# Performance work log

Measured on AMD Instinct MI355X. Metric: run time of the kernel, lower is better.

## Reference

```python
import jax, jax.numpy as jnp
import numpy as np

D = 512       # model_dim
H = 8         # num_heads
DH = D // H   # dim_per_head
LN_EPS = 1e-5


def setup_inputs() -> dict:
    key = jax.random.key(0)
    ks = jax.random.split(key, 10)
    B, S = 2, 2048
    s = D ** -0.5
    return {
        "query": jax.random.normal(ks[0], (B, S, D), jnp.float32),
        "key":   jax.random.normal(ks[1], (B, S, D), jnp.float32),
        "value": jax.random.normal(ks[2], (B, S, D), jnp.float32),
        # torch Linear weights: [out, in], y = x @ W.T
        "Wq": jax.random.normal(ks[3], (D, D), jnp.float32) * s,
        "Wk": jax.random.normal(ks[4], (D, D), jnp.float32) * s,
        "Wv": jax.random.normal(ks[5], (D, D), jnp.float32) * s,
        "Wo": jax.random.normal(ks[6], (D, D), jnp.float32) * s,
        "bo": jnp.zeros((D,), jnp.float32),
        "gamma": jnp.ones((D,), jnp.float32),
        "beta":  jnp.zeros((D,), jnp.float32),
    }


def _layer_norm(x, gamma, beta):
    mu = jnp.mean(x, axis=-1, keepdims=True)
    var = jnp.var(x, axis=-1, keepdims=True)
    return (x - mu) * jax.lax.rsqrt(var + LN_EPS) * gamma + beta


def reference(query, key, value, Wq, Wk, Wv, Wo, bo, gamma, beta):
    B, S, _ = query.shape
    residual = query
    # projections (torch Linear: x @ W.T), split heads -> [B, H, S, DH]
    q = (query @ Wq.T).reshape(B, S, H, DH).transpose(0, 2, 1, 3)
    k = (key   @ Wk.T).reshape(B, S, H, DH).transpose(0, 2, 1, 3)
    v = (value @ Wv.T).reshape(B, S, H, DH).transpose(0, 2, 1, 3)
    scale = DH ** -0.5
    scores = jnp.einsum('bhqd,bhkd->bhqk', q, k) * scale
    attention = jax.nn.softmax(scores, axis=-1)
    context = jnp.einsum('bhqk,bhkd->bhqd', attention, v)
    context = context.transpose(0, 2, 1, 3).reshape(B, S, D)
    output = context @ Wo.T + bo
    output = _layer_norm(residual + output, gamma, beta)
    # original returns attention as [B*H, S, S]
    return output, attention.reshape(B * H, S, S)
```

## Files before the change

### kernel.cpp

```cpp
#include <hip/hip_runtime.h>

#define B_ 2
#define S_ 2048
#define D_ 512
#define H_ 8
#define DH_ 64

typedef __bf16 bf16_8 __attribute__((ext_vector_type(8)));
typedef float f32x4 __attribute__((ext_vector_type(4)));
typedef unsigned int u32x4 __attribute__((ext_vector_type(4)));

union BfPack4 { ushort4 u; __bf16 h[4]; };

__global__ __launch_bounds__(256) void proj_qkv(
    const float* __restrict__ Xq, const float* __restrict__ Xk, const float* __restrict__ Xv,
    const float* __restrict__ Wq, const float* __restrict__ Wk, const float* __restrict__ Wv,
    __bf16* __restrict__ Qb, __bf16* __restrict__ Kb, __bf16* __restrict__ Vt)
{
    const int z = blockIdx.z;
    const float* X = (z == 0) ? Xq : (z == 1) ? Xk : Xv;
    const float* W = (z == 0) ? Wq : (z == 1) ? Wk : Wv;
    const int m0 = blockIdx.x * 64;
    const int n0 = blockIdx.y * 64;

    __shared__ __bf16 Xs[64][72];
    __shared__ __bf16 Ws[64][72];

    const int tid = threadIdx.x;
    const int w = tid >> 6, lane = tid & 63;
    const int quad = lane >> 4, mc = lane & 15;

    int rr[4], cc[4];
    for (int i = 0; i < 4; ++i) { int e = tid + i * 256; rr[i] = e >> 4; cc[i] = (e & 15) * 4; }

    f32x4 acc[4] = {};
    float4 xr[4], wv[4];
    for (int i = 0; i < 4; ++i) {
        xr[i] = *reinterpret_cast<const float4*>(&X[(size_t)(m0 + rr[i]) * 512 + cc[i]]);
        wv[i] = *reinterpret_cast<const float4*>(&W[(size_t)(n0 + rr[i]) * 512 + cc[i]]);
    }

    for (int kc = 0; kc < 512; kc += 64) {
        if (kc) __syncthreads();
        for (int i = 0; i < 4; ++i) {
            BfPack4 px, pw;
            px.h[0] = (__bf16)xr[i].x; px.h[1] = (__bf16)xr[i].y;
            px.h[2] = (__bf16)xr[i].z; px.h[3] = (__bf16)xr[i].w;
            *reinterpret_cast<ushort4*>(&Xs[rr[i]][cc[i]]) = px.u;
            pw.h[0] = (__bf16)wv[i].x; pw.h[1] = (__bf16)wv[i].y;
            pw.h[2] = (__bf16)wv[i].z; pw.h[3] = (__bf16)wv[i].w;
            *reinterpret_cast<ushort4*>(&Ws[rr[i]][cc[i]]) = pw.u;
        }
        __syncthreads();
        if (kc < 448) {
            for (int i = 0; i < 4; ++i) {
                xr[i] = *reinterpret_cast<const float4*>(&X[(size_t)(m0 + rr[i]) * 512 + kc + 64 + cc[i]]);
                wv[i] = *reinterpret_cast<const float4*>(&W[(size_t)(n0 + rr[i]) * 512 + kc + 64 + cc[i]]);
            }
        }
        for (int ks = 0; ks < 64; ks += 32) {
            bf16_8 a = *reinterpret_cast<const bf16_8*>(&Xs[w * 16 + mc][ks + quad * 8]);
            for (int tt = 0; tt < 4; ++tt) {
                bf16_8 bb = *reinterpret_cast<const bf16_8*>(&Ws[tt * 16 + mc][ks + quad * 8]);
                acc[tt] = __builtin_amdgcn_mfma_f32_16x16x32_bf16(a, bb, acc[tt], 0, 0, 0);
            }
        }
    }
    __syncthreads();
    const float scale = (z == 0) ? 0.125f : 1.0f;
    if (z < 2) {
        for (int tt = 0; tt < 4; ++tt)
            for (int r = 0; r < 4; ++r)
                Xs[w * 16 + quad * 4 + r][tt * 16 + mc] = (__bf16)(acc[tt][r] * scale);
    } else {
        for (int tt = 0; tt < 4; ++tt)
            for (int r = 0; r < 4; ++r)
                Xs[tt * 16 + mc][w * 16 + quad * 4 + r] = (__bf16)acc[tt][r];
    }
    __syncthreads();
    if (z < 2) {
        __bf16* out = (z == 0) ? Qb : Kb;
        for (int i = 0; i < 2; ++i) {
            int e = tid + i * 256;
            int r = e >> 3, c8 = (e & 7) * 8;
            *reinterpret_cast<uint4*>(&out[(size_t)(m0 + r) * 512 + n0 + c8]) =
                *reinterpret_cast<const uint4*>(&Xs[r][c8]);
        }
    } else {
        int b = m0 >> 11, s0 = m0 & 2047, h = n0 >> 6;
        for (int i = 0; i < 2; ++i) {
            int e = tid + i * 256;
            int r = e >> 3, c8 = (e & 7) * 8;
            *reinterpret_cast<uint4*>(&Vt[(((size_t)(b * H_ + h)) * DH_ + r) * S_ + s0 + c8]) =
                *reinterpret_cast<const uint4*>(&Xs[r][c8]);
        }
    }
}

__global__ __launch_bounds__(256) void attn_kernel(
    const __bf16* __restrict__ Qb, const __bf16* __restrict__ Kb, const __bf16* __restrict__ Vt,
    __bf16* __restrict__ Ctx, float* __restrict__ attn_out)
{
    const int qt = blockIdx.x;
    const int bh = blockIdx.y;
    const int b = bh >> 3, h = bh & 7;
    const int q0 = qt * 16;

    __shared__ __align__(16) char smem[4 * 16 * 528 * 2];
    __shared__ float Lsh[4][16];

    const int tid = threadIdx.x;
    const int kg = tid >> 6, lane = tid & 63;
    const int quad = lane >> 4, mc = lane & 15;

    __bf16* PsW = reinterpret_cast<__bf16*>(smem) + (size_t)kg * 16 * 528;

    const __bf16* qrow = &Qb[((size_t)b * S_ + q0 + mc) * D_ + h * DH_];
    const bf16_8 aq0 = *reinterpret_cast<const bf16_8*>(&qrow[quad * 8]);
    const bf16_8 aq1 = *reinterpret_cast<const bf16_8*>(&qrow[32 + quad * 8]);

    const __bf16* kbase = Kb + ((size_t)b * S_ + kg * 512) * D_ + h * DH_;
    const __bf16* vbase = Vt + (size_t)bh * DH_ * S_ + kg * 512;

    float l[4] = {0.f, 0.f, 0.f, 0.f};
    f32x4 o[4] = {};

    for (int c = 0; c < 8; ++c) {
        const __bf16* kc_ = kbase + (size_t)c * 64 * D_;
        bf16_8 kb[8];
        for (int tt = 0; tt < 4; ++tt)
            kb[tt] = *reinterpret_cast<const bf16_8*>(&kc_[(size_t)(tt * 16 + mc) * D_ + quad * 8]);
        for (int tt = 0; tt < 4; ++tt)
            kb[4 + tt] = *reinterpret_cast<const bf16_8*>(&kc_[(size_t)(tt * 16 + mc) * D_ + 32 + quad * 8]);
        f32x4 s[4] = {};
        for (int tt = 0; tt < 4; ++tt)
            s[tt] = __builtin_amdgcn_mfma_f32_16x16x32_bf16(aq0, kb[tt], s[tt], 0, 0, 0);
        for (int tt = 0; tt < 4; ++tt)
            s[tt] = __builtin_amdgcn_mfma_f32_16x16x32_bf16(aq1, kb[4 + tt], s[tt], 0, 0, 0);
        for (int tt = 0; tt < 4; ++tt)
            for (int j = 0; j < 4; ++j) {
                float p = __expf(s[tt][j]);
                l[j] += p;
                PsW[(size_t)(quad * 4 + j) * 528 + c * 64 + tt * 16 + mc] = (__bf16)p;
            }
        bf16_8 vb[8];
        for (int ks2 = 0; ks2 < 2; ++ks2)
            for (int tt = 0; tt < 4; ++tt)
                vb[ks2 * 4 + tt] = *reinterpret_cast<const bf16_8*>(
                    &vbase[(size_t)(tt * 16 + mc) * S_ + c * 64 + ks2 * 32 + quad * 8]);
        for (int ks2 = 0; ks2 < 2; ++ks2) {
            bf16_8 ap = *reinterpret_cast<const bf16_8*>(&PsW[(size_t)mc * 528 + c * 64 + ks2 * 32 + quad * 8]);
            for (int tt = 0; tt < 4; ++tt)
                o[tt] = __builtin_amdgcn_mfma_f32_16x16x32_bf16(ap, vb[ks2 * 4 + tt], o[tt], 0, 0, 0);
        }
    }

    for (int j = 0; j < 4; ++j)
        for (int off = 1; off < 16; off <<= 1) l[j] += __shfl_xor(l[j], off);
    if (mc == 0)
        for (int j = 0; j < 4; ++j) Lsh[kg][quad * 4 + j] = l[j];
    __syncthreads();

    for (int row = 0; row < 16; ++row) {
        const float li = 1.f / (Lsh[0][row] + Lsh[1][row] + Lsh[2][row] + Lsh[3][row]);
        u32x4 pv = *reinterpret_cast<const u32x4*>(&PsW[(size_t)row * 528 + lane * 8]);
        const __bf16* pp = reinterpret_cast<const __bf16*>(&pv);
        f32x4 lo, hi;
        for (int j = 0; j < 4; ++j) {
            lo[j] = (float)pp[j] * li;
            hi[j] = (float)pp[j + 4] * li;
        }
        float* dst = &attn_out[((size_t)bh * S_ + q0 + row) * S_ + kg * 512 + lane * 8];
        __builtin_nontemporal_store(lo, reinterpret_cast<f32x4*>(dst));
        __builtin_nontemporal_store(hi, reinterpret_cast<f32x4*>(dst + 4));
    }
    __syncthreads();

    float* Osc = reinterpret_cast<float*>(smem);
    for (int tt = 0; tt < 4; ++tt)
        for (int j = 0; j < 4; ++j)
            Osc[(size_t)kg * 16 * 68 + (quad * 4 + j) * 68 + tt * 16 + mc] = o[tt][j];
    __syncthreads();
    {
        const int row = tid >> 4;
        const int dhg = (tid & 15) * 4;
        const float li = 1.f / (Lsh[0][row] + Lsh[1][row] + Lsh[2][row] + Lsh[3][row]);
        BfPack4 pk;
        for (int kk = 0; kk < 4; ++kk) {
            float v = Osc[(size_t)0 * 16 * 68 + row * 68 + dhg + kk]
                    + Osc[(size_t)1 * 16 * 68 + row * 68 + dhg + kk]
                    + Osc[(size_t)2 * 16 * 68 + row * 68 + dhg + kk]
                    + Osc[(size_t)3 * 16 * 68 + row * 68 + dhg + kk];
            pk.h[kk] = (__bf16)(v * li);
        }
        *reinterpret_cast<ushort4*>(&Ctx[((size_t)b * S_ + q0 + row) * D_ + h * DH_ + dhg]) = pk.u;
    }
}

__global__ __launch_bounds__(256) void oproj(
    const __bf16* __restrict__ Ctx, const float* __restrict__ Wo,
    const float* __restrict__ bo, const float* __restrict__ resid,
    float* __restrict__ Y)
{
    const int m0 = blockIdx.x * 64;
    const int n0 = blockIdx.y * 64;

    __shared__ __bf16 As[64][72];
    __shared__ __bf16 Bs[64][72];

    const int tid = threadIdx.x;
    const int w = tid >> 6, lane = tid & 63;
    const int quad = lane >> 4, mc = lane & 15;

    int ar[2], ac[2], wr2[4], wc2[4];
    for (int i = 0; i < 2; ++i) { int e = tid + i * 256; ar[i] = e >> 3; ac[i] = (e & 7) * 8; }
    for (int i = 0; i < 4; ++i) { int e = tid + i * 256; wr2[i] = e >> 4; wc2[i] = (e & 15) * 4; }

    uint4 areg[2];
    float4 wreg[4];
    for (int i = 0; i < 2; ++i)
        areg[i] = *reinterpret_cast<const uint4*>(&Ctx[(size_t)(m0 + ar[i]) * 512 + ac[i]]);
    for (int i = 0; i < 4; ++i)
        wreg[i] = *reinterpret_cast<const float4*>(&Wo[(size_t)(n0 + wr2[i]) * 512 + wc2[i]]);

    f32x4 acc[4] = {};
    for (int kc = 0; kc < 512; kc += 64) {
        if (kc) __syncthreads();
        for (int i = 0; i < 2; ++i)
            *reinterpret_cast<uint4*>(&As[ar[i]][ac[i]]) = areg[i];
        for (int i = 0; i < 4; ++i) {
            BfPack4 pw;
            pw.h[0] = (__bf16)wreg[i].x; pw.h[1] = (__bf16)wreg[i].y;
            pw.h[2] = (__bf16)wreg[i].z; pw.h[3] = (__bf16)wreg[i].w;
            *reinterpret_cast<ushort4*>(&Bs[wr2[i]][wc2[i]]) = pw.u;
        }
        __syncthreads();
        if (kc < 448) {
            for (int i = 0; i < 2; ++i)
                areg[i] = *reinterpret_cast<const uint4*>(&Ctx[(size_t)(m0 + ar[i]) * 512 + kc + 64 + ac[i]]);
            for (int i = 0; i < 4; ++i)
                wreg[i] = *reinterpret_cast<const float4*>(&Wo[(size_t)(n0 + wr2[i]) * 512 + kc + 64 + wc2[i]]);
        }
        for (int ks = 0; ks < 64; ks += 32) {
            bf16_8 a = *reinterpret_cast<const bf16_8*>(&As[w * 16 + mc][ks + quad * 8]);
            for (int tt = 0; tt < 4; ++tt) {
                bf16_8 bb = *reinterpret_cast<const bf16_8*>(&Bs[tt * 16 + mc][ks + quad * 8]);
                acc[tt] = __builtin_amdgcn_mfma_f32_16x16x32_bf16(a, bb, acc[tt], 0, 0, 0);
            }
        }
    }
    for (int tt = 0; tt < 4; ++tt) {
        int col = n0 + tt * 16 + mc;
        float bias = bo[col];
        for (int r = 0; r < 4; ++r) {
            int row = m0 + w * 16 + quad * 4 + r;
            Y[(size_t)row * 512 + col] = acc[tt][r] + bias + resid[(size_t)row * 512 + col];
        }
    }
}

__global__ __launch_bounds__(256) void ln_kernel(
    const float* __restrict__ Y, const float* __restrict__ gamma,
    const float* __restrict__ beta, float* __restrict__ out)
{
    const int row = blockIdx.x * 4 + (threadIdx.x >> 6);
    const int lane = threadIdx.x & 63;
    const float* y = &Y[(size_t)row * 512];
    float4 v0 = *reinterpret_cast<const float4*>(&y[lane * 8]);
    float4 v1 = *reinterpret_cast<const float4*>(&y[lane * 8 + 4]);
    float sum = v0.x + v0.y + v0.z + v0.w + v1.x + v1.y + v1.z + v1.w;
    float sq = v0.x * v0.x + v0.y * v0.y + v0.z * v0.z + v0.w * v0.w +
               v1.x * v1.x + v1.y * v1.y + v1.z * v1.z + v1.w * v1.w;
    for (int off = 1; off < 64; off <<= 1) {
        sum += __shfl_xor(sum, off);
        sq  += __shfl_xor(sq, off);
    }
    const float mean = sum * (1.f / 512.f);
    const float var = sq * (1.f / 512.f) - mean * mean;
    const float rstd = rsqrtf(var + 1e-5f);
    float4 g0 = *reinterpret_cast<const float4*>(&gamma[lane * 8]);
    float4 g1 = *reinterpret_cast<const float4*>(&gamma[lane * 8 + 4]);
    float4 b0 = *reinterpret_cast<const float4*>(&beta[lane * 8]);
    float4 b1 = *reinterpret_cast<const float4*>(&beta[lane * 8 + 4]);
    float4 o0, o1;
    o0.x = (v0.x - mean) * rstd * g0.x + b0.x;
    o0.y = (v0.y - mean) * rstd * g0.y + b0.y;
    o0.z = (v0.z - mean) * rstd * g0.z + b0.z;
    o0.w = (v0.w - mean) * rstd * g0.w + b0.w;
    o1.x = (v1.x - mean) * rstd * g1.x + b1.x;
    o1.y = (v1.y - mean) * rstd * g1.y + b1.y;
    o1.z = (v1.z - mean) * rstd * g1.z + b1.z;
    o1.w = (v1.w - mean) * rstd * g1.w + b1.w;
    *reinterpret_cast<float4*>(&out[(size_t)row * 512 + lane * 8]) = o0;
    *reinterpret_cast<float4*>(&out[(size_t)row * 512 + lane * 8 + 4]) = o1;
}

extern "C" void kernel_launch(void* const* d_in, const int* in_sizes, int n_in,
                              void* d_out, int out_size, void* d_ws, size_t ws_size,
                              hipStream_t stream)
{
    const float* query = (const float*)d_in[0];
    const float* key   = (const float*)d_in[1];
    const float* value = (const float*)d_in[2];
    const float* Wq    = (const float*)d_in[3];
    const float* Wk    = (const float*)d_in[4];
    const float* Wv    = (const float*)d_in[5];
    const float* Wo    = (const float*)d_in[6];
    const float* bo    = (const float*)d_in[7];
    const float* gamma = (const float*)d_in[8];
    const float* beta  = (const float*)d_in[9];

    float* out = (float*)d_out;
    float* attn_out = out + (size_t)B_ * S_ * D_;

    char* ws = (char*)d_ws;
    __bf16* Qb  = (__bf16*)(ws);
    __bf16* Kb  = (__bf16*)(ws + (4u << 20));
    __bf16* Vt  = (__bf16*)(ws + (8u << 20));
    __bf16* Ctx = (__bf16*)(ws + (12u << 20));
    float*  Y   = (float*)(ws + (16u << 20));

    proj_qkv<<<dim3(64, 8, 3), 256, 0, stream>>>(query, key, value, Wq, Wk, Wv, Qb, Kb, Vt);
    attn_kernel<<<dim3(128, 16), 256, 0, stream>>>(Qb, Kb, Vt, Ctx, attn_out);
    oproj<<<dim3(64, 8), 256, 0, stream>>>(Ctx, Wo, bo, query, Y);
    ln_kernel<<<1024, 256, 0, stream>>>(Y, gamma, beta, out);
}
```

Measured before the change: 474.7 us.

## Split attention keys across eight waves and prefetch K/V one chunk ahead

The attention block grows from 4 to 8 wavefronts, so each wave handles 256 keys instead of 512, giving more parallel work and more waves per block to hide latency. The K/V loads for the next 64-key chunk are issued before the current chunk's MFMA work finishes, forming a software pipeline. Softmax denominators are reduced once into shared memory. In exchange there are more partial-output reductions across 8 groups and higher register pressure from the prefetch, constrained by the launch bounds of 512 threads with a minimum of 4 blocks.

```diff
diff --git a/kernel.cpp b/kernel.cpp
--- a/kernel.cpp
+++ b/kernel.cpp
@@ -97,7 +97,7 @@
     }
 }
 
-__global__ __launch_bounds__(256) void attn_kernel(
+__global__ __launch_bounds__(512, 4) void attn_kernel(
     const __bf16* __restrict__ Qb, const __bf16* __restrict__ Kb, const __bf16* __restrict__ Vt,
     __bf16* __restrict__ Ctx, float* __restrict__ attn_out)
 {
@@ -106,53 +106,64 @@
     const int b = bh >> 3, h = bh & 7;
     const int q0 = qt * 16;
 
-    __shared__ __align__(16) char smem[4 * 16 * 528 * 2];
-    __shared__ float Lsh[4][16];
+    __shared__ __align__(16) char smem[8 * 16 * 264 * 2];
+    __shared__ float Lsh[8][16];
+    __shared__ float linv_s[16];
 
     const int tid = threadIdx.x;
     const int kg = tid >> 6, lane = tid & 63;
     const int quad = lane >> 4, mc = lane & 15;
 
-    __bf16* PsW = reinterpret_cast<__bf16*>(smem) + (size_t)kg * 16 * 528;
+    __bf16* PsW = reinterpret_cast<__bf16*>(smem) + kg * 16 * 264;
 
     const __bf16* qrow = &Qb[((size_t)b * S_ + q0 + mc) * D_ + h * DH_];
     const bf16_8 aq0 = *reinterpret_cast<const bf16_8*>(&qrow[quad * 8]);
     const bf16_8 aq1 = *reinterpret_cast<const bf16_8*>(&qrow[32 + quad * 8]);
 
-    const __bf16* kbase = Kb + ((size_t)b * S_ + kg * 512) * D_ + h * DH_;
-    const __bf16* vbase = Vt + (size_t)bh * DH_ * S_ + kg * 512;
+    const __bf16* kbase = Kb + ((size_t)b * S_ + kg * 256) * D_ + h * DH_;
+    const __bf16* vbase = Vt + (size_t)bh * DH_ * S_ + kg * 256;
 
     float l[4] = {0.f, 0.f, 0.f, 0.f};
     f32x4 o[4] = {};
-
-    for (int c = 0; c < 8; ++c) {
-        const __bf16* kc_ = kbase + (size_t)c * 64 * D_;
-        bf16_8 kb[8];
-        for (int tt = 0; tt < 4; ++tt)
-            kb[tt] = *reinterpret_cast<const bf16_8*>(&kc_[(size_t)(tt * 16 + mc) * D_ + quad * 8]);
-        for (int tt = 0; tt < 4; ++tt)
-            kb[4 + tt] = *reinterpret_cast<const bf16_8*>(&kc_[(size_t)(tt * 16 + mc) * D_ + 32 + quad * 8]);
-        f32x4 s[4] = {};
-        for (int tt = 0; tt < 4; ++tt)
-            s[tt] = __builtin_amdgcn_mfma_f32_16x16x32_bf16(aq0, kb[tt], s[tt], 0, 0, 0);
-        for (int tt = 0; tt < 4; ++tt)
-            s[tt] = __builtin_amdgcn_mfma_f32_16x16x32_bf16(aq1, kb[4 + tt], s[tt], 0, 0, 0);
-        for (int tt = 0; tt < 4; ++tt)
-            for (int j = 0; j < 4; ++j) {
-                float p = __expf(s[tt][j]);
-                l[j] += p;
-                PsW[(size_t)(quad * 4 + j) * 528 + c * 64 + tt * 16 + mc] = (__bf16)p;
-            }
-        bf16_8 vb[8];
+    bf16_8 kb[8], vb[8];
+
+    auto loadK = [&](int c) {
+        for (int tt = 0; tt < 4; ++tt) {
+            const __bf16* kr = &kbase[(size_t)(c * 64 + tt * 16 + mc) * D_];
+            kb[tt]     = *reinterpret_cast<const bf16_8*>(&kr[quad * 8]);
+            kb[4 + tt] = *reinterpret_cast<const bf16_8*>(&kr[32 + quad * 8]);
+        }
+    };
+    auto loadV = [&](int c) {
         for (int ks2 = 0; ks2 < 2; ++ks2)
             for (int tt = 0; tt < 4; ++tt)
                 vb[ks2 * 4 + tt] = *reinterpret_cast<const bf16_8*>(
                     &vbase[(size_t)(tt * 16 + mc) * S_ + c * 64 + ks2 * 32 + quad * 8]);
+    };
+
+    loadK(0);
+    loadV(0);
+#pragma unroll
+    for (int c = 0; c < 4; ++c) {
+        f32x4 s[4] = {};
+        for (int tt = 0; tt < 4; ++tt)
+            s[tt] = __builtin_amdgcn_mfma_f32_16x16x32_bf16(aq0, kb[tt], s[tt], 0, 0, 0);
+        for (int tt = 0; tt < 4; ++tt)
+            s[tt] = __builtin_amdgcn_mfma_f32_16x16x32_bf16(aq1, kb[4 + tt], s[tt], 0, 0, 0);
+        for (int tt = 0; tt < 4; ++tt)
+            for (int j = 0; j < 4; ++j) {
+                float p = __expf(s[tt][j]);
+                l[j] += p;
+                PsW[(quad * 4 + j) * 264 + c * 64 + tt * 16 + mc] = (__bf16)p;
+            }
+        if (c < 3) loadK(c + 1);
         for (int ks2 = 0; ks2 < 2; ++ks2) {
-            bf16_8 ap = *reinterpret_cast<const bf16_8*>(&PsW[(size_t)mc * 528 + c * 64 + ks2 * 32 + quad * 8]);
+            bf16_8 ap = *reinterpret_cast<const bf16_8*>(
+                &PsW[mc * 264 + c * 64 + ks2 * 32 + quad * 8]);
             for (int tt = 0; tt < 4; ++tt)
                 o[tt] = __builtin_amdgcn_mfma_f32_16x16x32_bf16(ap, vb[ks2 * 4 + tt], o[tt], 0, 0, 0);
         }
+        if (c < 3) loadV(c + 1);
     }
 
     for (int j = 0; j < 4; ++j)
@@ -160,37 +171,38 @@
     if (mc == 0)
         for (int j = 0; j < 4; ++j) Lsh[kg][quad * 4 + j] = l[j];
     __syncthreads();
-
-    for (int row = 0; row < 16; ++row) {
-        const float li = 1.f / (Lsh[0][row] + Lsh[1][row] + Lsh[2][row] + Lsh[3][row]);
-        u32x4 pv = *reinterpret_cast<const u32x4*>(&PsW[(size_t)row * 528 + lane * 8]);
-        const __bf16* pp = reinterpret_cast<const __bf16*>(&pv);
-        f32x4 lo, hi;
-        for (int j = 0; j < 4; ++j) {
-            lo[j] = (float)pp[j] * li;
-            hi[j] = (float)pp[j + 4] * li;
-        }
-        float* dst = &attn_out[((size_t)bh * S_ + q0 + row) * S_ + kg * 512 + lane * 8];
-        __builtin_nontemporal_store(lo, reinterpret_cast<f32x4*>(dst));
-        __builtin_nontemporal_store(hi, reinterpret_cast<f32x4*>(dst + 4));
+    if (tid < 16) {
+        float t = 0.f;
+        for (int g = 0; g < 8; ++g) t += Lsh[g][tid];
+        linv_s[tid] = 1.f / t;
+    }
+    __syncthreads();
+
+    for (int r = 0; r < 16; ++r) {
+        const float li = linv_s[r];
+        BfPack4 pu;
+        pu.u = *reinterpret_cast<const ushort4*>(&PsW[r * 264 + lane * 4]);
+        f32x4 ov;
+        for (int j = 0; j < 4; ++j) ov[j] = (float)pu.h[j] * li;
+        __builtin_nontemporal_store(ov, reinterpret_cast<f32x4*>(
+            &attn_out[((size_t)bh * S_ + q0 + r) * S_ + kg * 256 + lane * 4]));
     }
     __syncthreads();
 
     float* Osc = reinterpret_cast<float*>(smem);
     for (int tt = 0; tt < 4; ++tt)
         for (int j = 0; j < 4; ++j)
-            Osc[(size_t)kg * 16 * 68 + (quad * 4 + j) * 68 + tt * 16 + mc] = o[tt][j];
-    __syncthreads();
-    {
+            Osc[(kg * 16 + quad * 4 + j) * 68 + tt * 16 + mc] = o[tt][j];
+    __syncthreads();
+    if (tid < 256) {
         const int row = tid >> 4;
         const int dhg = (tid & 15) * 4;
-        const float li = 1.f / (Lsh[0][row] + Lsh[1][row] + Lsh[2][row] + Lsh[3][row]);
+        const float li = linv_s[row];
         BfPack4 pk;
         for (int kk = 0; kk < 4; ++kk) {
-            float v = Osc[(size_t)0 * 16 * 68 + row * 68 + dhg + kk]
-                    + Osc[(size_t)1 * 16 * 68 + row * 68 + dhg + kk]
-                    + Osc[(size_t)2 * 16 * 68 + row * 68 + dhg + kk]
-                    + Osc[(size_t)3 * 16 * 68 + row * 68 + dhg + kk];
+            float v = 0.f;
+            for (int g = 0; g < 8; ++g)
+                v += Osc[(g * 16 + row) * 68 + dhg + kk];
             pk.h[kk] = (__bf16)(v * li);
         }
         *reinterpret_cast<ushort4*>(&Ctx[((size_t)b * S_ + q0 + row) * D_ + h * DH_ + dhg]) = pk.u;
@@ -321,7 +333,7 @@
     float*  Y   = (float*)(ws + (16u << 20));
 
     proj_qkv<<<dim3(64, 8, 3), 256, 0, stream>>>(query, key, value, Wq, Wk, Wv, Qb, Kb, Vt);
-    attn_kernel<<<dim3(128, 16), 256, 0, stream>>>(Qb, Kb, Vt, Ctx, attn_out);
+    attn_kernel<<<dim3(128, 16), 512, 0, stream>>>(Qb, Kb, Vt, Ctx, attn_out);
     oproj<<<dim3(64, 8), 256, 0, stream>>>(Ctx, Wo, bo, query, Y);
     ln_kernel<<<1024, 256, 0, stream>>>(Y, gamma, beta, out);
 }
```

Result: faster. 449.7 us (-5.3%).
